# Performance work log

Measured on AMD Instinct MI355X. Metric: run time of the kernel, lower is better.

The kernel has to match this reference:

```python
import jax, jax.numpy as jnp
import numpy as np

FRAME_RATE = 2048
B, T, L = 64, 256, 65536


def setup_inputs() -> dict:
    key = jax.random.key(0)
    ks = jax.random.split(key, 20)
    F = FRAME_RATE
    s = 0.05
    return {
        "alpha": jnp.sort(jax.random.randint(ks[0], (B, T), 0, L), axis=1).astype(jnp.int32),
        "sound": jax.random.normal(ks[1], (B, L), jnp.float32),
        "conv1_w": jax.random.normal(ks[2], (F - 2,), jnp.float32) * s,
        "conv1_b": jax.random.normal(ks[3], (1,), jnp.float32) * s,
        "conv2_w": jax.random.normal(ks[4], (32, 1, 3), jnp.float32) * s,
        "conv2_b": jax.random.normal(ks[5], (32,), jnp.float32) * s,
        "conv3_w": jax.random.normal(ks[6], (128, 32, 3), jnp.float32) * s,
        "conv3_b": jax.random.normal(ks[7], (128,), jnp.float32) * s,
        "lin_w": jax.random.normal(ks[8], (256, 129), jnp.float32) * s,
        "lin_b": jax.random.normal(ks[9], (256,), jnp.float32) * s,
        "w_ih": jax.random.normal(ks[10], (1024, 256), jnp.float32) * s,
        "w_hh": jax.random.normal(ks[11], (1024, 256), jnp.float32) * s,
        "b_ih": jax.random.normal(ks[12], (1024,), jnp.float32) * s,
        "b_hh": jax.random.normal(ks[13], (1024,), jnp.float32) * s,
        "out1_w": jax.random.normal(ks[14], (32, 256), jnp.float32) * s,
        "out1_b": jax.random.normal(ks[15], (32,), jnp.float32) * s,
        "out2_w": jax.random.normal(ks[16], (1, 32), jnp.float32) * s,
        "out2_b": jax.random.normal(ks[17], (1,), jnp.float32) * s,
    }


def reference(alpha, sound, conv1_w, conv1_b, conv2_w, conv2_b, conv3_w, conv3_b,
              lin_w, lin_b, w_ih, w_hh, b_ih, b_hh, out1_w, out1_b, out2_w, out2_b):
    F = conv1_w.shape[0] + 2  # frame_rate
    Bsz, Tlen = alpha.shape
    pad = F // 2
    # Vectorized gather of all per-timestep fragments (replaces nested python loops).
    padded = jnp.pad(sound, ((0, 0), (pad, pad)))               # [B, L + 2*(F//2)]
    idx = alpha[:, :, None] + jnp.arange(F)[None, None, :]      # [B, T, F]
    frags = jnp.take_along_axis(padded[:, None, :], idx, axis=2)  # [B, T, F]
    frags = frags.transpose(1, 0, 2)                            # [T, B, F]
    K = F - 2
    # conv1: 1->1 channel, kernel F-2, output length 3 (three big dot products)
    y1 = jnp.stack([jnp.einsum('tbf,f->tb', frags[:, :, i:i + K], conv1_w)
                    for i in range(3)], axis=-1) + conv1_b[0]   # [T, B, 3]
    # conv2: 1->32 channels, kernel 3, padding 1 (output length stays 3), then ReLU
    y1p = jnp.pad(y1, ((0, 0), (0, 0), (1, 1)))
    win = jnp.stack([y1p[:, :, l:l + 3] for l in range(3)], axis=2)  # [T, B, 3(l), 3(k)]
    y2 = jax.nn.relu(jnp.einsum('tblk,ck->tbcl', win, conv2_w[:, 0, :])
                     + conv2_b[None, None, :, None])            # [T, B, 32, 3]
    # conv3: 32->128 channels, kernel 3, no padding -> output length 1 (no relu, matching source)
    y3 = jnp.einsum('tbck,ock->tbo', y2, conv3_w) + conv3_b     # [T, B, 128]
    # interval = alpha_t - alpha_{t-1} (0 at t=0)
    prev = jnp.concatenate([jnp.zeros((Bsz, 1), alpha.dtype), alpha[:, :-1]], axis=1)
    interval = (alpha - prev).T.astype(frags.dtype)             # [T, B]
    x = jnp.concatenate([interval[..., None], y3], axis=-1)     # [T, B, 129]
    x = x @ lin_w.T + lin_b                                     # [T, B, 256]
    H = w_hh.shape[1]

    def step(carry, xt):
        h, c = carry
        g = xt @ w_ih.T + b_ih + h @ w_hh.T + b_hh              # [B, 4H]
        i_, f_, g_, o_ = jnp.split(g, 4, axis=-1)
        c = jax.nn.sigmoid(f_) * c + jax.nn.sigmoid(i_) * jnp.tanh(g_)
        h = jax.nn.sigmoid(o_) * jnp.tanh(c)
        return (h, c), None

    h0 = jnp.zeros((Bsz, H), x.dtype)
    (h, c), _ = jax.lax.scan(step, (h0, h0), x)
    ht = h[None]                                                # [1, B, 256]
    out = jax.nn.sigmoid(jax.nn.relu(ht @ out1_w.T + out1_b) @ out2_w.T + out2_b)
    return out                                                  # [1, B, 1]
```

## Files before the change

### kernel.cpp

```cpp
#include <hip/hip_runtime.h>
#include <math.h>

#define BSZ 64
#define TLEN 256
#define LSND 65536
#define ZK 160

typedef __attribute__((ext_vector_type(8))) short bf16x8;
typedef __attribute__((ext_vector_type(4))) float f32x4;

__device__ __forceinline__ float sigm(float x) { return 1.f / (1.f + __expf(-x)); }
__device__ __forceinline__ float tanh_f(float x) {
  float e = __expf(-2.f * fabsf(x));
  return copysignf((1.f - e) / (1.f + e), x);
}
__device__ __forceinline__ unsigned short f2bf(float x) {
  unsigned u = __float_as_uint(x);
  return (unsigned short)((u + 0x7FFFu + ((u >> 16) & 1u)) >> 16);
}
__device__ __forceinline__ f32x4 unpack4(unsigned long long v) {
  f32x4 r;
  r[0] = __uint_as_float((unsigned)(v & 0xFFFFu) << 16);
  r[1] = __uint_as_float((unsigned)((v >> 16) & 0xFFFFu) << 16);
  r[2] = __uint_as_float((unsigned)((v >> 32) & 0xFFFFu) << 16);
  r[3] = __uint_as_float((unsigned)((v >> 48) & 0xFFFFu) << 16);
  return r;
}
__device__ __forceinline__ int nrow(int q, int m) {
  return ((m & 3) << 8) + (q << 2) + (m >> 2);
}

__global__ __launch_bounds__(256) void prep_kernel(
    const float* __restrict__ w_ih, const float* __restrict__ lin_w,
    const float* __restrict__ lin_b, const float* __restrict__ b_ih,
    const float* __restrict__ b_hh, float* __restrict__ Wc, float* __restrict__ bc)
{
  __shared__ float sRow[256];
  const int n = blockIdx.x;
  const int j = threadIdx.x;
  sRow[j] = w_ih[n * 256 + j];
  __syncthreads();
  if (j < 132) {
    float acc = 0.f;
    if (j < 129) {
      for (int k = 0; k < 256; ++k) acc += sRow[k] * lin_w[k * 129 + j];
    }
    Wc[n * 132 + j] = acc;
  } else if (j == 255) {
    float acc = b_ih[n] + b_hh[n];
    for (int k = 0; k < 256; ++k) acc += sRow[k] * lin_b[k];
    bc[n] = acc;
  }
}

__global__ __launch_bounds__(256) void transpose_w3(const float* __restrict__ w3,
                                                    float* __restrict__ w3t)
{
  int i = blockIdx.x * 256 + threadIdx.x;
  if (i < 96 * 128) { int s = i >> 7, o = i & 127; w3t[i] = w3[o * 96 + s]; }
}

__global__ __launch_bounds__(256) void pack_wc(
    const float* __restrict__ Wc, const float* __restrict__ bc,
    unsigned short* __restrict__ Wcperm, float* __restrict__ bcp)
{
  const int cid = blockIdx.x * 256 + threadIdx.x;
  if (cid >= 64 * 5 * 64) return;
  const int q = cid / 320, rem = cid - q * 320;
  const int o = rem >> 6, l = rem & 63;
  const int m = l >> 2, kg = l & 3;
  const int n = nrow(q, m);
  unsigned short out[8];
  #pragma unroll
  for (int e = 0; e < 8; ++e) {
    const int kz = o * 32 + kg * 8 + e;
    float v = (kz < 129) ? Wc[n * 132 + kz] : (kz == 129 ? Wc[n * 132] : 0.f);
    out[e] = f2bf(v);
  }
  *(ulonglong2*)(Wcperm + cid * 8) = *(ulonglong2*)out;
  if (o == 0 && kg == 0) bcp[q * 16 + m] = bc[n];
}

__global__ __launch_bounds__(256) void pack_whh(
    const float* __restrict__ whh, unsigned short* __restrict__ whhp)
{
  const int cid = blockIdx.x * 256 + threadIdx.x;
  const int q = cid >> 9, rem = cid & 511;
  const int o = rem >> 6, l = rem & 63;
  const int m = l >> 2, kg = l & 3;
  const int n = nrow(q, m);
  unsigned short out[8];
  #pragma unroll
  for (int e = 0; e < 8; ++e)
    out[e] = f2bf(whh[n * 256 + o * 32 + kg * 8 + e]);
  *(ulonglong2*)(whhp + cid * 8) = *(ulonglong2*)out;
}

__global__ __launch_bounds__(64) void conv_kernel(
    const int* __restrict__ alpha, const float* __restrict__ sound,
    const float* __restrict__ w1, const float* __restrict__ b1v,
    const float* __restrict__ w2, const float* __restrict__ b2,
    const float* __restrict__ w3t, const float* __restrict__ b3,
    unsigned short* __restrict__ zw)
{
  __shared__ float win[2048];
  __shared__ float sY2[96];
  const int l = threadIdx.x;
  const int b = blockIdx.x >> 8;
  const int t = blockIdx.x & 255;
  const int a = alpha[b * TLEN + t];
  const int a0 = a - 1024;
  const float* srow = sound + (size_t)b * LSND;
  for (int x = l; x < 2048; x += 64) {
    int p = a0 + x;
    win[x] = (p >= 0 && p < LSND) ? srow[p] : 0.f;
  }
  __syncthreads();
  float acc0 = 0.f, acc1 = 0.f, acc2 = 0.f;
  for (int f = l; f < 2046; f += 64) {
    float wv = w1[f];
    acc0 += win[f] * wv;
    acc1 += win[f + 1] * wv;
    acc2 += win[f + 2] * wv;
  }
  for (int m = 32; m; m >>= 1) {
    acc0 += __shfl_xor(acc0, m);
    acc1 += __shfl_xor(acc1, m);
    acc2 += __shfl_xor(acc2, m);
  }
  const float bb = b1v[0];
  const float y11 = acc0 + bb, y12 = acc1 + bb, y13 = acc2 + bb;
  {
    int s = l;
    int c = s / 3, lp = s - c * 3;
    float wA = w2[c * 3], wB = w2[c * 3 + 1], wC = w2[c * 3 + 2];
    float v = (lp == 0) ? (y11 * wB + y12 * wC)
            : (lp == 1) ? (y11 * wA + y12 * wB + y13 * wC)
                        : (y12 * wA + y13 * wB);
    sY2[s] = fmaxf(v + b2[c], 0.f);
    if (l < 32) {
      s = 64 + l; c = s / 3; lp = s - c * 3;
      wA = w2[c * 3]; wB = w2[c * 3 + 1]; wC = w2[c * 3 + 2];
      v = (lp == 0) ? (y11 * wB + y12 * wC)
        : (lp == 1) ? (y11 * wA + y12 * wB + y13 * wC)
                    : (y12 * wA + y13 * wB);
      sY2[s] = fmaxf(v + b2[c], 0.f);
    }
  }
  __syncthreads();
  float o0 = b3[l], o1 = b3[l + 64];
  for (int s = 0; s < 96; ++s) {
    float yv = sY2[s];
    o0 += yv * w3t[s * 128 + l];
    o1 += yv * w3t[s * 128 + l + 64];
  }
  unsigned short* zrow = zw + ((size_t)t * BSZ + b) * ZK;
  zrow[1 + l] = f2bf(o0);
  zrow[65 + l] = f2bf(o1);
  if (l == 0) {
    int prev = (t > 0) ? alpha[b * TLEN + t - 1] : 0;
    float iv = (float)(a - prev);
    unsigned short hi = f2bf(iv);
    zrow[0] = hi;
    float rec = __uint_as_float(((unsigned)hi) << 16);
    zrow[129] = f2bf(iv - rec);
  }
  if (l < 30) zrow[130 + l] = 0;
}

__global__ __launch_bounds__(256) void xw_gemm(
    const unsigned short* __restrict__ zw, const unsigned short* __restrict__ Wcperm,
    const float* __restrict__ bcp, unsigned short* __restrict__ xwp)
{
  const int t = (int)blockIdx.x >> 2;
  const int bt = (int)blockIdx.x & 3;
  const int tid = threadIdx.x;
  const int w = tid >> 6, ln = tid & 63;
  const int bl = ln & 15, kg = ln >> 4;

  bf16x8 zf[5];
  #pragma unroll
  for (int o = 0; o < 5; ++o)
    zf[o] = *(const bf16x8*)(zw + ((size_t)t * BSZ + (bt << 4) + bl) * ZK + o * 32 + kg * 8);

  #pragma unroll 2
  for (int qq = 0; qq < 16; ++qq) {
    const int q = (w << 4) + qq;
    f32x4 acc = *(const f32x4*)(bcp + q * 16 + (kg << 2));
    #pragma unroll
    for (int o = 0; o < 5; ++o) {
      bf16x8 af = *(const bf16x8*)(Wcperm + ((size_t)(q * 5 + o) * 64 + (bl << 2) + kg) * 8);
      acc = __builtin_amdgcn_mfma_f32_16x16x32_bf16(af, zf[o], acc, 0, 0, 0);
    }
    uint2 pk;
    pk.x = (unsigned)f2bf(acc[0]) | ((unsigned)f2bf(acc[1]) << 16);
    pk.y = (unsigned)f2bf(acc[2]) | ((unsigned)f2bf(acc[3]) << 16);
    char* dst = (char*)xwp + (((size_t)t * 4 + bt) << 15)
              + ((q * 32 + bl * 2 + (kg >> 1)) << 4) + ((kg & 1) << 3);
    *(uint2*)dst = pk;
  }
}

__global__ void __launch_bounds__(512, 1) lstm_kernel(
    const unsigned short* __restrict__ whhp, const unsigned short* __restrict__ xwp,
    unsigned long long* __restrict__ hq, float* __restrict__ hfin)
{
  __shared__ unsigned short sH[2][16][256];
  char* sHb = (char*)sH;

  const int tid = threadIdx.x;
  const int w = tid >> 6, ln = tid & 63;
  const int bl = ln & 15, kg = ln >> 4;
  const int bid = (int)blockIdx.x;
  const int bt = bid >> 1, jh = bid & 1;
  const int b = (bt << 4) + bl;
  const int pb = (jh ^ 1) << 7;

  bf16x8 wfr[4][8];
  #pragma unroll
  for (int q = 0; q < 4; ++q) {
    const int qg = (jh << 5) + (w << 2) + q;
    #pragma unroll
    for (int o = 0; o < 8; ++o)
      wfr[q][o] = *(const bf16x8*)(whhp + (((size_t)(qg * 8 + o) * 16 + bl) * 4 + kg) * 8);
  }

  for (int i = tid; i < 4096; i += 512) ((unsigned*)sHb)[i] = 0;

  const int prow = tid >> 5;
  const int pj0 = pb + ((tid & 31) << 2);
  char* pdst = sHb + (prow << 9) + (((pj0 >> 3) ^ prow) << 4) + ((pj0 & 7) << 1);
  float cs[4] = {0.f, 0.f, 0.f, 0.f};

  #pragma unroll 1
  for (int t = 0; t < TLEN; ++t) {
    const int p_ = (t & 1) << 13;

    unsigned long long xwv[4];
    {
      const char* xb = (const char*)xwp + (((size_t)t * 4 + bt) << 15) + ((kg & 1) << 3);
      #pragma unroll
      for (int q = 0; q < 4; ++q) {
        const int chunk = (((jh << 5) + (w << 2) + q) << 5) + (bl << 1) + (kg >> 1);
        xwv[q] = *(const unsigned long long*)(xb + (chunk << 4));
      }
    }

    if (t > 0) {
      const unsigned long long* hs =
          hq + ((size_t)(t & 1)) * 8192 + ((size_t)(bid ^ 1) << 10) + (tid << 1);
      const unsigned tagw = (unsigned)t;
      unsigned long long v0 =
          __hip_atomic_load(hs, __ATOMIC_RELAXED, __HIP_MEMORY_SCOPE_AGENT);
      unsigned long long v1 =
          __hip_atomic_load(hs + 1, __ATOMIC_RELAXED, __HIP_MEMORY_SCOPE_AGENT);
      int guard = 0;
      for (;;) {
        bool ok = true;
        if ((unsigned)(v0 >> 32) != tagw) {
          v0 = __hip_atomic_load(hs, __ATOMIC_RELAXED, __HIP_MEMORY_SCOPE_AGENT);
          ok = false;
        }
        if ((unsigned)(v1 >> 32) != tagw) {
          v1 = __hip_atomic_load(hs + 1, __ATOMIC_RELAXED, __HIP_MEMORY_SCOPE_AGENT);
          ok = false;
        }
        if (ok || ++guard > (1 << 20)) break;
      }
      uint2 pay;
      pay.x = (unsigned)v0;
      pay.y = (unsigned)v1;
      *(uint2*)(pdst + p_) = pay;
    }
    __syncthreads();

    bf16x8 hf[8];
    #pragma unroll
    for (int o = 0; o < 8; ++o)
      hf[o] = *(const bf16x8*)(sHb + p_ + (bl << 9) + ((((o << 2) + kg) ^ bl) << 4));

    #pragma unroll
    for (int q = 0; q < 4; ++q) {
      f32x4 acc = unpack4(xwv[q]);
      #pragma unroll
      for (int o = 0; o < 8; ++o)
        acc = __builtin_amdgcn_mfma_f32_16x16x32_bf16(wfr[q][o], hf[o], acc, 0, 0, 0);
      cs[q] = sigm(acc[1]) * cs[q] + sigm(acc[0]) * tanh_f(acc[2]);
      const float hv = sigm(acc[3]) * tanh_f(cs[q]);
      const float hp = __shfl_xor(hv, 16);
      const int jloc = (w << 4) + (q << 2) + kg;
      const int jglob = (jh << 7) + jloc;
      if (t < TLEN - 1) {
        if (!(kg & 1)) {
          const unsigned d = (unsigned)f2bf(hv) | ((unsigned)f2bf(hp) << 16);
          *(unsigned*)(sHb + (p_ ^ 8192) + (bl << 9)
                       + (((jglob >> 3) ^ bl) << 4) + ((jglob & 7) << 1)) = d;
          const unsigned long long pk =
              ((unsigned long long)(unsigned)(t + 1) << 32) | d;
          __hip_atomic_store(hq + ((size_t)((t + 1) & 1)) * 8192 + ((size_t)bid << 10)
                                 + (bl << 6) + (jloc >> 1),
                             pk, __ATOMIC_RELAXED, __HIP_MEMORY_SCOPE_AGENT);
        }
      } else {
        hfin[b * 256 + jglob] = hv;
      }
    }
  }
}

__global__ __launch_bounds__(256) void head_kernel(
    const float* __restrict__ hfin, const float* __restrict__ o1w,
    const float* __restrict__ o1b, const float* __restrict__ o2w,
    const float* __restrict__ o2b, float* __restrict__ out)
{
  __shared__ float sR[32];
  const int b = blockIdx.x;
  const int tid = threadIdx.x;
  const int m = tid >> 3, g = tid & 7;
  const float* h = hfin + b * 256;
  float acc = 0.f;
  for (int k = g * 32; k < g * 32 + 32; ++k) acc += h[k] * o1w[m * 256 + k];
  acc += __shfl_xor(acc, 1); acc += __shfl_xor(acc, 2); acc += __shfl_xor(acc, 4);
  if (g == 0) sR[m] = fmaxf(acc + o1b[m], 0.f);
  __syncthreads();
  if (tid == 0) {
    float s = o2b[0];
    for (int mm = 0; mm < 32; ++mm) s += sR[mm] * o2w[mm];
    out[b] = sigm(s);
  }
}

extern "C" void kernel_launch(void* const* d_in, const int* in_sizes, int n_in,
                              void* d_out, int out_size, void* d_ws, size_t ws_size,
                              hipStream_t stream) {
  (void)in_sizes; (void)n_in; (void)out_size; (void)ws_size;
  const int*   alpha = (const int*)  d_in[0];
  const float* sound = (const float*)d_in[1];
  const float* w1    = (const float*)d_in[2];
  const float* b1    = (const float*)d_in[3];
  const float* w2    = (const float*)d_in[4];
  const float* b2    = (const float*)d_in[5];
  const float* w3    = (const float*)d_in[6];
  const float* b3    = (const float*)d_in[7];
  const float* linw  = (const float*)d_in[8];
  const float* linb  = (const float*)d_in[9];
  const float* wih   = (const float*)d_in[10];
  const float* whh   = (const float*)d_in[11];
  const float* bih   = (const float*)d_in[12];
  const float* bhh   = (const float*)d_in[13];
  const float* o1w   = (const float*)d_in[14];
  const float* o1b   = (const float*)d_in[15];
  const float* o2w   = (const float*)d_in[16];
  const float* o2b   = (const float*)d_in[17];

  char* p = (char*)d_ws;
  unsigned short* zw     = (unsigned short*)p;
  float*          Wc     = (float*)(p + 5242880);
  float*          bc     = (float*)(p + 5783552);
  float*          w3t    = (float*)(p + 5787648);
  float*          hfin   = (float*)(p + 5836800);
  unsigned short* Wcperm = (unsigned short*)(p + 5902336);
  float*          bcp    = (float*)(p + 6230016);
  unsigned short* whhp   = (unsigned short*)(p + 6234112);
  unsigned short* xwp    = (unsigned short*)(p + 6758400);
  unsigned long long* hq = (unsigned long long*)(p + 5902336);

  prep_kernel<<<1024, 256, 0, stream>>>(wih, linw, linb, bih, bhh, Wc, bc);
  transpose_w3<<<48, 256, 0, stream>>>(w3, w3t);
  conv_kernel<<<BSZ * TLEN, 64, 0, stream>>>(alpha, sound, w1, b1, w2, b2, w3t, b3, zw);
  pack_wc<<<80, 256, 0, stream>>>(Wc, bc, Wcperm, bcp);
  pack_whh<<<128, 256, 0, stream>>>(whh, whhp);
  xw_gemm<<<TLEN * 4, 256, 0, stream>>>(zw, Wcperm, bcp, xwp);
  hipMemsetAsync(hq, 0, 131072, stream);
  lstm_kernel<<<8, 512, 0, stream>>>(whhp, xwp, hq, hfin);
  head_kernel<<<BSZ, 256, 0, stream>>>(hfin, o1w, o1b, o2w, o2b, (float*)d_out);
}
```

Baseline: 989.6 us.

## Overlap own-half recurrent MFMAs with partner handoff polling and prefetch xw

```diff
diff --git a/kernel.cpp b/kernel.cpp
--- a/kernel.cpp
+++ b/kernel.cpp
@@ -203,7 +203,7 @@
 
 __global__ void __launch_bounds__(512, 1) lstm_kernel(
     const unsigned short* __restrict__ whhp, const unsigned short* __restrict__ xwp,
-    unsigned long long* __restrict__ hq, float* __restrict__ hfin)
+    unsigned* __restrict__ hq, float* __restrict__ hfin)
 {
   __shared__ unsigned short sH[2][16][256];
   char* sHb = (char*)sH;
@@ -214,6 +214,8 @@
   const int bid = (int)blockIdx.x;
   const int bt = bid >> 1, jh = bid & 1;
   const int b = (bt << 4) + bl;
+  const int oOwn = jh << 2;
+  const int oPar = (jh ^ 1) << 2;
   const int pb = (jh ^ 1) << 7;
 
   bf16x8 wfr[4][8];
@@ -228,83 +230,117 @@
   for (int i = tid; i < 4096; i += 512) ((unsigned*)sHb)[i] = 0;
 
   const int prow = tid >> 5;
-  const int pj0 = pb + ((tid & 31) << 2);
-  char* pdst = sHb + (prow << 9) + (((pj0 >> 3) ^ prow) << 4) + ((pj0 & 7) << 1);
+  const int pj0 = (tid & 31) << 2;
+  const unsigned pollidx = (unsigned)(prow * 128 + pj0);
+  char* pdst = sHb + (prow << 9) + ((((pb + pj0) >> 3) ^ prow) << 4) + ((pj0 & 7) << 1);
+
+  unsigned long long xcur[4], xnxt[4];
+  {
+    const char* xb = (const char*)xwp + (((size_t)0 * 4 + bt) << 15) + ((kg & 1) << 3);
+    #pragma unroll
+    for (int q = 0; q < 4; ++q) {
+      const int chunk = (((jh << 5) + (w << 2) + q) << 5) + (bl << 1) + (kg >> 1);
+      xcur[q] = *(const unsigned long long*)(xb + (chunk << 4));
+    }
+  }
   float cs[4] = {0.f, 0.f, 0.f, 0.f};
+  __syncthreads();
 
   #pragma unroll 1
   for (int t = 0; t < TLEN; ++t) {
     const int p_ = (t & 1) << 13;
 
-    unsigned long long xwv[4];
+    f32x4 acc[4];
     {
-      const char* xb = (const char*)xwp + (((size_t)t * 4 + bt) << 15) + ((kg & 1) << 3);
+      bf16x8 hfo[4];
+      #pragma unroll
+      for (int o = 0; o < 4; ++o)
+        hfo[o] = *(const bf16x8*)(sHb + p_ + (bl << 9)
+                                  + (((((oOwn + o) << 2) + kg) ^ bl) << 4));
+      #pragma unroll
+      for (int q = 0; q < 4; ++q) {
+        acc[q] = unpack4(xcur[q]);
+        #pragma unroll
+        for (int o = 0; o < 4; ++o)
+          acc[q] = __builtin_amdgcn_mfma_f32_16x16x32_bf16(wfr[q][oOwn + o], hfo[o],
+                                                           acc[q], 0, 0, 0);
+      }
+    }
+    if (t + 1 < TLEN) {
+      const char* xb = (const char*)xwp + (((size_t)(t + 1) * 4 + bt) << 15) + ((kg & 1) << 3);
       #pragma unroll
       for (int q = 0; q < 4; ++q) {
         const int chunk = (((jh << 5) + (w << 2) + q) << 5) + (bl << 1) + (kg >> 1);
-        xwv[q] = *(const unsigned long long*)(xb + (chunk << 4));
+        xnxt[q] = *(const unsigned long long*)(xb + (chunk << 4));
       }
     }
 
     if (t > 0) {
-      const unsigned long long* hs =
-          hq + ((size_t)(t & 1)) * 8192 + ((size_t)(bid ^ 1) << 10) + (tid << 1);
-      const unsigned tagw = (unsigned)t;
-      unsigned long long v0 =
-          __hip_atomic_load(hs, __ATOMIC_RELAXED, __HIP_MEMORY_SCOPE_AGENT);
-      unsigned long long v1 =
-          __hip_atomic_load(hs + 1, __ATOMIC_RELAXED, __HIP_MEMORY_SCOPE_AGENT);
+      const unsigned* hs = hq + ((size_t)(t & 1)) * 16384
+                         + ((size_t)(bid ^ 1) << 11) + pollidx;
+      const unsigned tagw = (unsigned)t & 0xFFFFu;
+      unsigned v0 = __hip_atomic_load(hs + 0, __ATOMIC_RELAXED, __HIP_MEMORY_SCOPE_AGENT);
+      unsigned v1 = __hip_atomic_load(hs + 1, __ATOMIC_RELAXED, __HIP_MEMORY_SCOPE_AGENT);
+      unsigned v2 = __hip_atomic_load(hs + 2, __ATOMIC_RELAXED, __HIP_MEMORY_SCOPE_AGENT);
+      unsigned v3 = __hip_atomic_load(hs + 3, __ATOMIC_RELAXED, __HIP_MEMORY_SCOPE_AGENT);
       int guard = 0;
       for (;;) {
         bool ok = true;
-        if ((unsigned)(v0 >> 32) != tagw) {
-          v0 = __hip_atomic_load(hs, __ATOMIC_RELAXED, __HIP_MEMORY_SCOPE_AGENT);
-          ok = false;
-        }
-        if ((unsigned)(v1 >> 32) != tagw) {
-          v1 = __hip_atomic_load(hs + 1, __ATOMIC_RELAXED, __HIP_MEMORY_SCOPE_AGENT);
-          ok = false;
-        }
+        if ((v0 & 0xFFFFu) != tagw) {
+          v0 = __hip_atomic_load(hs + 0, __ATOMIC_RELAXED, __HIP_MEMORY_SCOPE_AGENT); ok = false; }
+        if ((v1 & 0xFFFFu) != tagw) {
+          v1 = __hip_atomic_load(hs + 1, __ATOMIC_RELAXED, __HIP_MEMORY_SCOPE_AGENT); ok = false; }
+        if ((v2 & 0xFFFFu) != tagw) {
+          v2 = __hip_atomic_load(hs + 2, __ATOMIC_RELAXED, __HIP_MEMORY_SCOPE_AGENT); ok = false; }
+        if ((v3 & 0xFFFFu) != tagw) {
+          v3 = __hip_atomic_load(hs + 3, __ATOMIC_RELAXED, __HIP_MEMORY_SCOPE_AGENT); ok = false; }
         if (ok || ++guard > (1 << 20)) break;
       }
-      uint2 pay;
-      pay.x = (unsigned)v0;
-      pay.y = (unsigned)v1;
-      *(uint2*)(pdst + p_) = pay;
+      unsigned long long pay =
+          (unsigned long long)(v0 >> 16)
+        | ((unsigned long long)(v1 >> 16) << 16)
+        | ((unsigned long long)(v2 >> 16) << 32)
+        | ((unsigned long long)(v3 >> 16) << 48);
+      *(unsigned long long*)(pdst + p_) = pay;
     }
     __syncthreads();
 
-    bf16x8 hf[8];
-    #pragma unroll
-    for (int o = 0; o < 8; ++o)
-      hf[o] = *(const bf16x8*)(sHb + p_ + (bl << 9) + ((((o << 2) + kg) ^ bl) << 4));
+    {
+      bf16x8 hfp[4];
+      #pragma unroll
+      for (int o = 0; o < 4; ++o)
+        hfp[o] = *(const bf16x8*)(sHb + p_ + (bl << 9)
+                                  + (((((oPar + o) << 2) + kg) ^ bl) << 4));
+      #pragma unroll
+      for (int q = 0; q < 4; ++q) {
+        #pragma unroll
+        for (int o = 0; o < 4; ++o)
+          acc[q] = __builtin_amdgcn_mfma_f32_16x16x32_bf16(wfr[q][oPar + o], hfp[o],
+                                                           acc[q], 0, 0, 0);
+      }
+    }
 
     #pragma unroll
     for (int q = 0; q < 4; ++q) {
-      f32x4 acc = unpack4(xwv[q]);
-      #pragma unroll
-      for (int o = 0; o < 8; ++o)
-        acc = __builtin_amdgcn_mfma_f32_16x16x32_bf16(wfr[q][o], hf[o], acc, 0, 0, 0);
-      cs[q] = sigm(acc[1]) * cs[q] + sigm(acc[0]) * tanh_f(acc[2]);
-      const float hv = sigm(acc[3]) * tanh_f(cs[q]);
-      const float hp = __shfl_xor(hv, 16);
+      cs[q] = sigm(acc[q][1]) * cs[q] + sigm(acc[q][0]) * tanh_f(acc[q][2]);
+      const float hv = sigm(acc[q][3]) * tanh_f(cs[q]);
       const int jloc = (w << 4) + (q << 2) + kg;
       const int jglob = (jh << 7) + jloc;
       if (t < TLEN - 1) {
-        if (!(kg & 1)) {
-          const unsigned d = (unsigned)f2bf(hv) | ((unsigned)f2bf(hp) << 16);
-          *(unsigned*)(sHb + (p_ ^ 8192) + (bl << 9)
-                       + (((jglob >> 3) ^ bl) << 4) + ((jglob & 7) << 1)) = d;
-          const unsigned long long pk =
-              ((unsigned long long)(unsigned)(t + 1) << 32) | d;
-          __hip_atomic_store(hq + ((size_t)((t + 1) & 1)) * 8192 + ((size_t)bid << 10)
-                                 + (bl << 6) + (jloc >> 1),
-                             pk, __ATOMIC_RELAXED, __HIP_MEMORY_SCOPE_AGENT);
-        }
+        const unsigned short hb = f2bf(hv);
+        const unsigned pk = ((unsigned)hb << 16) | ((unsigned)(t + 1) & 0xFFFFu);
+        __hip_atomic_store(hq + ((size_t)((t + 1) & 1)) * 16384 + ((size_t)bid << 11)
+                               + (bl << 7) + jloc,
+                           pk, __ATOMIC_RELAXED, __HIP_MEMORY_SCOPE_AGENT);
+        *(unsigned short*)(sHb + (p_ ^ 8192) + (bl << 9)
+                           + (((jglob >> 3) ^ bl) << 4) + ((jglob & 7) << 1)) = hb;
       } else {
         hfin[b * 256 + jglob] = hv;
       }
     }
+    #pragma unroll
+    for (int q = 0; q < 4; ++q) xcur[q] = xnxt[q];
+    __syncthreads();
   }
 }
 
@@ -363,7 +399,7 @@
   float*          bcp    = (float*)(p + 6230016);
   unsigned short* whhp   = (unsigned short*)(p + 6234112);
   unsigned short* xwp    = (unsigned short*)(p + 6758400);
-  unsigned long long* hq = (unsigned long long*)(p + 5902336);
+  unsigned*       hq     = (unsigned*)(p + 5902336);
 
   prep_kernel<<<1024, 256, 0, stream>>>(wih, linw, linb, bih, bhh, Wc, bc);
   transpose_w3<<<48, 256, 0, stream>>>(w3, w3t);
```

Measured after the change: 2.661 ms. 169% more time.
